# Performance work log

Hardware: AMD Instinct MI355X
Metric: run time of the kernel (lower is better)

The kernel has to match this reference:

```python
import math
import jax, jax.numpy as jnp
import numpy as np

K = 1.0            # Lorentz manifold curvature k
B, S = 4, 2048     # batch, seq_len
IN, H, OUT = 512, 8, 64   # in_channels, num_heads, out_channels (space dim; head_dim = OUT+1)


def setup_inputs() -> dict:
    key = jax.random.key(0)
    ks = jax.random.split(key, 8)
    std = 1.0 / math.sqrt(IN)
    return {
        "query_input": jax.random.normal(ks[0], (B, S, IN), jnp.float32),
        "source_input": jax.random.normal(ks[1], (B, S, IN), jnp.float32),
        # per-head HypLinear weights stacked on a leading head axis: [H, OUT, IN]
        "Wq_w": jax.random.normal(ks[2], (H, OUT, IN), jnp.float32) * std,
        "Wq_b": jnp.zeros((H, OUT), jnp.float32),
        "Wk_w": jax.random.normal(ks[3], (H, OUT, IN), jnp.float32) * std,
        "Wk_b": jnp.zeros((H, OUT), jnp.float32),
        "Wv_w": jax.random.normal(ks[4], (H, OUT, IN), jnp.float32) * std,
        "Wv_b": jnp.zeros((H, OUT), jnp.float32),
        "scale": jnp.array([math.sqrt(OUT)], jnp.float32),  # nn.Parameter([sqrt(out_channels)])
        "bias": jnp.zeros((), jnp.float32),                 # nn.Parameter(zeros(()))
    }


def hyp_linear(x, w, b):
    # HypLinear: linear map to space part, recompute Lorentz time coord sqrt(||x_s||^2 + k)
    sp = jnp.einsum('bsi,hoi->bsho', x, w) + b            # [B,S,H,OUT]
    t = jnp.sqrt(jnp.sum(sp * sp, axis=-1, keepdims=True) + K)
    return jnp.concatenate([t, sp], axis=-1)              # [B,S,H,OUT+1]


def reference(query_input, source_input, Wq_w, Wq_b, Wk_w, Wk_b, Wv_w, Wv_b, scale, bias):
    q = hyp_linear(query_input, Wq_w, Wq_b)   # [B,S,H,D], D = OUT+1
    k = hyp_linear(source_input, Wk_w, Wk_b)
    v = hyp_linear(source_input, Wv_w, Wv_b)

    # Lorentzian cinner: <x,y>_L = -x0*y0 + <x_s, y_s>
    sgn = jnp.concatenate([-jnp.ones((1,), q.dtype), jnp.ones((OUT,), q.dtype)])
    att = jnp.einsum('bqhd,bkhd->bhqk', q * sgn, k)       # [B,H,S,S]
    att = (2.0 + 2.0 * att) / scale[0] + bias

    causal = jnp.triu(jnp.full((S, S), -1e9, q.dtype), 1)  # causal mask (additive)
    att = jax.nn.softmax(att + causal, axis=-1)

    ctx = jnp.einsum('bhqk,bkhd->bqhd', att, v)           # [B,S,H,D]

    # manifold.mid_point over the heads axis (dim=-2)
    ave = jnp.mean(ctx, axis=2)                           # [B,S,D]
    inner = -ave[..., :1] ** 2 + jnp.sum(ave[..., 1:] ** 2, axis=-1, keepdims=True)
    denom = jnp.sqrt(jnp.maximum(jnp.abs(-inner), 1e-8))
    return math.sqrt(K) * ave / denom                     # [B,S,D]
```

## Files before the change

kernel.cpp:

```cpp
#include <hip/hip_runtime.h>

#define BATCH 4
#define SEQ   2048
#define INC   512
#define NH    8
#define OUTC  64
#define DD    65
#define NROW  (BATCH * NH * SEQ)

typedef float f32x4 __attribute__((ext_vector_type(4)));
typedef short short8 __attribute__((ext_vector_type(8)));
typedef short short4v __attribute__((ext_vector_type(4)));
typedef unsigned int uint2v __attribute__((ext_vector_type(2)));
typedef unsigned short us;

static __device__ __forceinline__ us f2b(float f) {
  unsigned int u = __float_as_uint(f);
  u = (u + 0x7FFFu + ((u >> 16) & 1u)) >> 16;
  return (us)u;
}
static __device__ __forceinline__ float b2f(us h) {
  return __uint_as_float(((unsigned int)h) << 16);
}
static __device__ __forceinline__ unsigned int pk2(float lo, float hi) {
  unsigned int r;
  asm("v_cvt_pk_bf16_f32 %0, %1, %2" : "=v"(r) : "v"(lo), "v"(hi));
  return r;
}

#define GLDS(g, l) __builtin_amdgcn_global_load_lds( \
    (const __attribute__((address_space(1))) void*)(g), \
    (__attribute__((address_space(3))) void*)(l), 16, 0, 0)
#define SB() __builtin_amdgcn_sched_barrier(0)

__global__ __launch_bounds__(256) void tobf16_kernel(
    const float* __restrict__ Xq, const float* __restrict__ Xs,
    const float* __restrict__ Wq, const float* __restrict__ Wk,
    const float* __restrict__ Wv,
    us* __restrict__ dXq, us* __restrict__ dXs,
    us* __restrict__ dWq, us* __restrict__ dWk, us* __restrict__ dWv)
{
  const int which = blockIdx.y;
  const float* src;
  us* dst;
  int n;
  switch (which) {
    case 0: src = Xq; dst = dXq; n = BATCH * SEQ * INC; break;
    case 1: src = Xs; dst = dXs; n = BATCH * SEQ * INC; break;
    case 2: src = Wq; dst = dWq; n = NH * OUTC * INC; break;
    case 3: src = Wk; dst = dWk; n = NH * OUTC * INC; break;
    default: src = Wv; dst = dWv; n = NH * OUTC * INC; break;
  }
  for (long i = (long)blockIdx.x * 256 + threadIdx.x; i * 4 < n;
       i += (long)gridDim.x * 256) {
    f32x4 v = *(const f32x4*)(src + i * 4);
    short4v o;
    o[0] = (short)f2b(v[0]); o[1] = (short)f2b(v[1]);
    o[2] = (short)f2b(v[2]); o[3] = (short)f2b(v[3]);
    *(short4v*)(dst + i * 4) = o;
  }
}

__global__ __launch_bounds__(256) void proj_kernel(
    const us* __restrict__ Xqb, const us* __restrict__ Xsb,
    const us* __restrict__ Wqb, const us* __restrict__ Wkb, const us* __restrict__ Wvb,
    const float* __restrict__ Bq, const float* __restrict__ Bk, const float* __restrict__ Bv,
    const float* __restrict__ scale_p,
    us* __restrict__ qs, unsigned int* __restrict__ qta,
    us* __restrict__ ks, unsigned int* __restrict__ kta,
    us* __restrict__ vs, us* __restrict__ vtc)
{
  const int which = blockIdx.z;
  const us* X = (which == 0) ? Xqb : Xsb;
  const us* W = (which == 0) ? Wqb : (which == 1 ? Wkb : Wvb);
  const float* Bb = (which == 0) ? Bq : (which == 1 ? Bk : Bv);
  us* outs = (which == 0) ? qs : (which == 1 ? ks : vs);
  const float al2 = (2.0f / scale_p[0]) * 1.44269504088896f;
  const float oscale = (which == 0) ? al2 : 1.0f;

  const int lin = blockIdx.x;
  const int h   = (lin >> 3) & 7;
  const int m0  = (((lin >> 6) << 3) | (lin & 7)) * 64;
  const int n0  = h * 64;

  __shared__ alignas(16) us lX[2][64 * 64];
  __shared__ alignas(16) us lW[2][64 * 64];

  const int tid  = threadIdx.x;
  const int lane = tid & 63;
  const int wave = tid >> 6;
  const int arow = lane & 15;
  const int agrp = lane >> 4;
  const int rl   = lane >> 3;
  const int chx  = ((lane & 7) ^ rl) * 8;
  const int r0   = wave * 8 + rl;
  const int r1   = r0 + 32;

#define PSTAGE(buf, k0) do { \
    GLDS(X + (size_t)(m0 + r0) * INC + (k0) + chx, &lX[buf][wave * 512]); \
    GLDS(X + (size_t)(m0 + r1) * INC + (k0) + chx, &lX[buf][2048 + wave * 512]); \
    GLDS(W + (size_t)(n0 + r0) * INC + (k0) + chx, &lW[buf][wave * 512]); \
    GLDS(W + (size_t)(n0 + r1) * INC + (k0) + chx, &lW[buf][2048 + wave * 512]); \
  } while (0)

  f32x4 acc[4] = {};
  PSTAGE(0, 0);

  for (int kk = 0; kk < 8; ++kk) {
    const int cur = kk & 1;
    if (kk < 7) {
      PSTAGE(cur ^ 1, (kk + 1) * 64);
      asm volatile("s_waitcnt vmcnt(4)");
    } else {
      asm volatile("s_waitcnt vmcnt(0)");
    }
    __builtin_amdgcn_s_barrier();
#pragma unroll
    for (int kc = 0; kc < 2; ++kc) {
      short8 af = *(const short8*)&lX[cur][(wave * 16 + arow) * 64 + (((kc * 4 + agrp) ^ (arow & 7)) * 8)];
#pragma unroll
      for (int c = 0; c < 4; ++c) {
        short8 bf = *(const short8*)&lW[cur][(c * 16 + arow) * 64 + (((kc * 4 + agrp) ^ (arow & 7)) * 8)];
        acc[c] = __builtin_amdgcn_mfma_f32_16x16x32_bf16(af, bf, acc[c], 0, 0, 0);
      }
    }
    __builtin_amdgcn_s_barrier();
  }

  float bcol[4];
#pragma unroll
  for (int c = 0; c < 4; ++c) bcol[c] = Bb[n0 + c * 16 + arow];
#pragma unroll
  for (int r = 0; r < 4; ++r) {
    float s2 = 0.f;
#pragma unroll
    for (int c = 0; c < 4; ++c) {
      float v = acc[c][r] + bcol[c];
      acc[c][r] = v;
      s2 += v * v;
    }
    s2 += __shfl_xor(s2, 1); s2 += __shfl_xor(s2, 2);
    s2 += __shfl_xor(s2, 4); s2 += __shfl_xor(s2, 8);
    float tv = sqrtf(s2 + 1.0f);
    int gs = m0 + wave * 16 + agrp * 4 + r;
    int bi = gs >> 11, si = gs & (SEQ - 1);
    size_t rowbase = (size_t)(bi * NH + h) * SEQ + si;
    size_t obase = rowbase * 64;
#pragma unroll
    for (int c = 0; c < 4; ++c) outs[obase + c * 16 + arow] = f2b(oscale * acc[c][r]);
    if (arow == 0) {
      if (which == 0) {
        float st = al2 * tv;
        us qh = f2b(st);
        us ql = f2b(st - b2f(qh));
        qta[rowbase] = (unsigned int)qh | ((unsigned int)ql << 16);
      } else {
        us th = f2b(tv);
        us tl = f2b(tv - b2f(th));
        if (which == 1) {
          kta[rowbase] = (unsigned int)(us)(th ^ 0x8000)
                       | ((unsigned int)(us)(tl ^ 0x8000) << 16);
        } else {
          vtc[rowbase] = th;
          vtc[NROW + rowbase] = tl;
        }
      }
    }
  }
}

__global__ __launch_bounds__(256) void transpose_v_kernel(
    const us* __restrict__ vs, us* __restrict__ vT)
{
  const int bh = blockIdx.y;
  const int s0 = blockIdx.x * 64;
  __shared__ us lT[64 * 80];
  const int tid = threadIdx.x;
#pragma unroll
  for (int u0 = 0; u0 < 2; ++u0) {
    int u = tid + u0 * 256;
    int row = u >> 3, ch = u & 7;
    short8 v = *(const short8*)&vs[((size_t)bh * SEQ + s0 + row) * 64 + ch * 8];
    *(short8*)&lT[row * 80 + ch * 8] = v;
  }
  __syncthreads();
#pragma unroll
  for (int u0 = 0; u0 < 2; ++u0) {
    int u = tid + u0 * 256;
    int o = u >> 3, sc = u & 7;
    short8 w;
#pragma unroll
    for (int j = 0; j < 8; ++j) w[j] = lT[(sc * 8 + j) * 80 + o];
    *(short8*)&vT[((size_t)bh * 64 + o) * SEQ + s0 + sc * 8] = w;
  }
}

__global__ __launch_bounds__(512) void attn_kernel(
    const us* __restrict__ qs, const unsigned int* __restrict__ qta,
    const us* __restrict__ ks, const unsigned int* __restrict__ kta,
    const us* __restrict__ vT, const us* __restrict__ vtc,
    float* __restrict__ part)
{
  const int f = blockIdx.x;
  const int xcd = f & 7, idx = f >> 3;
  const int bh = xcd * 4 + (idx / 24);
  const int inner = idx % 24;
  const int x = inner / 3;
  const int s = inner % 3;
  const int n0 = 2 * x + 2;
  const int n1 = 32 - 2 * x;

  __shared__ alignas(16) us lK[2][64 * 64];
  __shared__ alignas(16) us lV[2][64 * 64];
  __shared__ alignas(16) us lP[8][16 * 40];

  const int tid  = threadIdx.x;
  const int lane = tid & 63;
  const int wave = tid >> 6;
  const int arow = lane & 15;
  const int agrp = lane >> 4;

  const size_t bhbase = (size_t)bh * SEQ;
  const us* kgp = ks + bhbase * 64;
  const us* vgp = vT + (size_t)bh * 64 * SEQ;
  const unsigned int* ktp = kta + bhbase;
  const us* vtp = vtc + (size_t)(arow & 1) * NROW + bhbase;

  const int rl   = lane >> 3;
  const int chx  = ((lane & 7) ^ rl) * 8;
  const int dsl0 = (agrp ^ (arow & 7)) * 8;
  const int dsl1 = ((4 + agrp) ^ (arow & 7)) * 8;
  us* myP = &lP[wave][0];
  const int pw0 = arow * 40 + agrp * 4;
  const int prd = arow * 40 + agrp * 8;

#define ASTAGE(buf, t64) do { \
    const int kk = (t64) * 64; \
    GLDS(kgp + (size_t)(kk + wave * 8 + rl) * 64 + chx, &lK[buf][wave * 512]); \
    GLDS(vgp + (size_t)(wave * 8 + rl) * SEQ + kk + chx, &lV[buf][wave * 512]); \
  } while (0)

  short8 ones8, zero8 = {};
#pragma unroll
  for (int j = 0; j < 8; ++j) ones8[j] = (short)0x3F80;

  for (int seg = 0; seg < 2; ++seg) {
    const int qT = seg ? (15 - x) : x;
    int lo, hi;
    if (seg == 0) { lo = min(12 * s, n0);          hi = min(12 * s + 12, n0); }
    else          { lo = max(12 * s - n0, 0);      hi = min(12 * s + 12 - n0, n1); }
    const int nt = hi - lo;
    if (nt <= 0) continue;

    const int wq = qT * 128 + wave * 16 + arow;
    f32x4 acc[5] = {};

    const us* qp = qs + (bhbase + wq) * 64;
    short8 qf0 = *(const short8*)(qp + agrp * 8);
    short8 qf1 = *(const short8*)(qp + 32 + agrp * 8);
    unsigned int qw = qta[bhbase + wq];
    short8 qf2 = {};
    if (agrp == 0) {
      qf2[0] = (short)(qw & 0xFFFFu);
      qf2[1] = (short)(qw & 0xFFFFu);
      qf2[2] = (short)(qw >> 16);
    }

    unsigned int ka[4];
    short8 va0, va1;
    {
      const int kk = lo * 64;
#pragma unroll
      for (int c = 0; c < 4; ++c) ka[c] = ktp[kk + c * 16 + arow];
      va0 = *(const short8*)(vtp + kk + agrp * 8);
      va1 = *(const short8*)(vtp + kk + 32 + agrp * 8);
    }
    SB();
    ASTAGE(0, lo);
    SB();

    for (int it = 0; it < nt; ++it) {
      const int t = lo + it;
      const int cur = it & 1;
      if (it < nt - 1) {
        ASTAGE(cur ^ 1, t + 1);
        SB();
        asm volatile("s_waitcnt vmcnt(2)");
      } else {
        SB();
        asm volatile("s_waitcnt vmcnt(0)");
      }
      SB();
      __builtin_amdgcn_s_barrier();

      const us* Kb = lK[cur];
      const us* Vb = lV[cur];

      f32x4 sS[4] = {};
      __builtin_amdgcn_s_setprio(1);
#pragma unroll
      for (int c = 0; c < 4; ++c) {
        short8 kf = *(const short8*)&Kb[(c * 16 + arow) * 64 + dsl0];
        sS[c] = __builtin_amdgcn_mfma_f32_16x16x32_bf16(kf, qf0, sS[c], 0, 0, 0);
      }
#pragma unroll
      for (int c = 0; c < 4; ++c) {
        short8 kf = *(const short8*)&Kb[(c * 16 + arow) * 64 + dsl1];
        sS[c] = __builtin_amdgcn_mfma_f32_16x16x32_bf16(kf, qf1, sS[c], 0, 0, 0);
      }
#pragma unroll
      for (int c = 0; c < 4; ++c) {
        short8 kf2 = {};
        if (agrp == 0) {
          unsigned int w0 = ka[c];
          kf2[0] = (short)(w0 & 0xFFFFu);
          kf2[1] = (short)(w0 >> 16);
          kf2[2] = (short)(w0 & 0xFFFFu);
        }
        sS[c] = __builtin_amdgcn_mfma_f32_16x16x32_bf16(kf2, qf2, sS[c], 0, 0, 0);
      }
      __builtin_amdgcn_s_setprio(0);

#pragma unroll
      for (int c = 0; c < 4; ++c)
#pragma unroll
        for (int r = 0; r < 4; ++r)
          sS[c][r] = exp2f(sS[c][r]);
      if (t >= 2 * qT) {
        const int kb = t * 64;
#pragma unroll
        for (int c = 0; c < 4; ++c)
#pragma unroll
          for (int r = 0; r < 4; ++r)
            if (kb + c * 16 + agrp * 4 + r > wq) sS[c][r] = 0.f;
      }

      {
        uint2v w;
        w[0] = pk2(sS[0][0], sS[0][1]); w[1] = pk2(sS[0][2], sS[0][3]);
        *(uint2v*)&myP[pw0] = w;
        w[0] = pk2(sS[1][0], sS[1][1]); w[1] = pk2(sS[1][2], sS[1][3]);
        *(uint2v*)&myP[pw0 + 16] = w;
        short8 pf = *(const short8*)&myP[prd];
        __builtin_amdgcn_s_setprio(1);
#pragma unroll
        for (int dc = 0; dc < 4; ++dc) {
          short8 vf = *(const short8*)&Vb[(dc * 16 + arow) * 64 + dsl0];
          acc[dc] = __builtin_amdgcn_mfma_f32_16x16x32_bf16(pf, vf, acc[dc], 0, 0, 0);
        }
        short8 vf4 = (arow < 2) ? va0 : ((arow == 2) ? ones8 : zero8);
        acc[4] = __builtin_amdgcn_mfma_f32_16x16x32_bf16(pf, vf4, acc[4], 0, 0, 0);
        __builtin_amdgcn_s_setprio(0);
      }
      {
        uint2v w;
        w[0] = pk2(sS[2][0], sS[2][1]); w[1] = pk2(sS[2][2], sS[2][3]);
        *(uint2v*)&myP[pw0] = w;
        w[0] = pk2(sS[3][0], sS[3][1]); w[1] = pk2(sS[3][2], sS[3][3]);
        *(uint2v*)&myP[pw0 + 16] = w;
        short8 pf = *(const short8*)&myP[prd];
        __builtin_amdgcn_s_setprio(1);
#pragma unroll
        for (int dc = 0; dc < 4; ++dc) {
          short8 vf = *(const short8*)&Vb[(dc * 16 + arow) * 64 + dsl1];
          acc[dc] = __builtin_amdgcn_mfma_f32_16x16x32_bf16(pf, vf, acc[dc], 0, 0, 0);
        }
        short8 vf4 = (arow < 2) ? va1 : ((arow == 2) ? ones8 : zero8);
        acc[4] = __builtin_amdgcn_mfma_f32_16x16x32_bf16(pf, vf4, acc[4], 0, 0, 0);
        __builtin_amdgcn_s_setprio(0);
      }

      SB();
      if (it + 1 < nt) {
        const int kk = (t + 1) * 64;
#pragma unroll
        for (int c = 0; c < 4; ++c) ka[c] = ktp[kk + c * 16 + arow];
        va0 = *(const short8*)(vtp + kk + agrp * 8);
        va1 = *(const short8*)(vtp + kk + 32 + agrp * 8);
      }
      SB();
      __builtin_amdgcn_s_barrier();
    }

    const size_t pb = ((size_t)(bh * 16 + qT) * 3 + s) * 128;
#pragma unroll
    for (int r = 0; r < 4; ++r) {
      float t0 = __shfl(acc[4][r], (agrp << 4) | 0);
      float t1 = __shfl(acc[4][r], (agrp << 4) | 1);
      float ls = __shfl(acc[4][r], (agrp << 4) | 2);
      size_t rp = (pb + wave * 16 + agrp * 4 + r) * 68;
#pragma unroll
      for (int dc = 0; dc < 4; ++dc)
        part[rp + dc * 16 + arow] = acc[dc][r];
      if (arow == 0) {
        part[rp + 64] = t0 + t1;
        part[rp + 65] = ls;
      }
    }
  }
}

__global__ __launch_bounds__(256) void finalize_kernel(
    const float* __restrict__ part, float* __restrict__ out)
{
  const int tid  = threadIdx.x;
  const int lane = tid & 63;
  const int gw = blockIdx.x * 4 + (tid >> 6);
  const int b = gw >> 11, si = gw & (SEQ - 1);
  const int qT = si >> 7, row = si & 127;

  const bool v0 = (qT <= 7) || (qT >= 11);
  const bool v1 = (qT >= 6);
  const bool v2 = (qT >= 8);

  float vsum = 0.f, tsum = 0.f;
#pragma unroll
  for (int h = 0; h < NH; ++h) {
    const size_t tb = ((size_t)(b * NH + h) * 16 + qT) * 3;
    float Ah = 0.f, Th = 0.f, Lh = 0.f;
    if (v0) {
      size_t rb = ((tb + 0) * 128 + row) * 68;
      Ah += part[rb + lane]; Th += part[rb + 64]; Lh += part[rb + 65];
    }
    if (v1) {
      size_t rb = ((tb + 1) * 128 + row) * 68;
      Ah += part[rb + lane]; Th += part[rb + 64]; Lh += part[rb + 65];
    }
    if (v2) {
      size_t rb = ((tb + 2) * 128 + row) * 68;
      Ah += part[rb + lane]; Th += part[rb + 64]; Lh += part[rb + 65];
    }
    float inv = 1.0f / Lh;
    vsum = fmaf(Ah, inv, vsum);
    tsum = fmaf(Th, inv, tsum);
  }
  float ave  = vsum * 0.125f;
  float tave = tsum * 0.125f;
  float contrib = ave * ave;
  if (lane == 0) contrib -= tave * tave;
  contrib += __shfl_xor(contrib, 1);
  contrib += __shfl_xor(contrib, 2);
  contrib += __shfl_xor(contrib, 4);
  contrib += __shfl_xor(contrib, 8);
  contrib += __shfl_xor(contrib, 16);
  contrib += __shfl_xor(contrib, 32);
  float denom = sqrtf(fmaxf(fabsf(contrib), 1e-8f));
  size_t ob = ((size_t)b * SEQ + si) * (size_t)DD;
  out[ob + 1 + lane] = ave / denom;
  if (lane == 0) out[ob] = tave / denom;
}

extern "C" void kernel_launch(void* const* d_in, const int* in_sizes, int n_in,
                              void* d_out, int out_size, void* d_ws, size_t ws_size,
                              hipStream_t stream) {
  const float* Xq  = (const float*)d_in[0];
  const float* Xs  = (const float*)d_in[1];
  const float* Wq  = (const float*)d_in[2];
  const float* Bq  = (const float*)d_in[3];
  const float* Wk  = (const float*)d_in[4];
  const float* Bk  = (const float*)d_in[5];
  const float* Wv  = (const float*)d_in[6];
  const float* Bv  = (const float*)d_in[7];
  const float* scale = (const float*)d_in[8];
  float* out = (float*)d_out;

  char* p = (char*)d_ws;

  float* part = (float*)p;
  us* Xqb   = (us*)p;
  us* Xsb   = (us*)(p + 16777216);
  us* Wqb16 = (us*)(p + 33554432);
  us* Wkb16 = (us*)(p + 34078720);
  us* Wvb16 = (us*)(p + 34603008);
  us* vsb   = (us*)(p + 35651584);
  p += (size_t)32 * 16 * 3 * 128 * 68 * 4;
  us* qsb = (us*)p; p += (size_t)NROW * 64 * 2;
  us* ksb = (us*)p; p += (size_t)NROW * 64 * 2;
  us* vTb = (us*)p; p += (size_t)NROW * 64 * 2;
  unsigned int* qtaw = (unsigned int*)p; p += (size_t)NROW * 4;
  unsigned int* ktaw = (unsigned int*)p; p += (size_t)NROW * 4;
  us* vtcw = (us*)p; p += (size_t)NROW * 2 * 2;

  tobf16_kernel<<<dim3(1024, 5), 256, 0, stream>>>(
      Xq, Xs, Wq, Wk, Wv, Xqb, Xsb, Wqb16, Wkb16, Wvb16);
  proj_kernel<<<dim3(1024, 1, 3), 256, 0, stream>>>(
      Xqb, Xsb, Wqb16, Wkb16, Wvb16, Bq, Bk, Bv, scale,
      qsb, qtaw, ksb, ktaw, vsb, vtcw);
  transpose_v_kernel<<<dim3(SEQ / 64, BATCH * NH), 256, 0, stream>>>(vsb, vTb);
  attn_kernel<<<dim3(768), 512, 0, stream>>>(
      qsb, qtaw, ksb, ktaw, vTb, vtcw, part);
  finalize_kernel<<<(BATCH * SEQ) / 4, 256, 0, stream>>>(part, out);
}
```

Baseline: 100.4 us.

## Fuse V transpose into projection kernel and store attention partials as bf16

The V projection blocks now stage their output tile in shared memory and write V already transposed, which removes the separate transpose kernel launch and the round trip of V through global memory. The attention partial context vectors are stored as bf16 with a 72-element stride, keeping the time and sum fields as fp32. This cuts the bytes written by the attention kernel and read by finalize. Storing partials in bf16 loses precision before the normalisation and cross-split sum.

Result: faster. 96.30 us, median of 2 (-4.1%).

```diff
diff --git a/kernel.cpp b/kernel.cpp
--- a/kernel.cpp
+++ b/kernel.cpp
@@ -7,6 +7,7 @@
 #define OUTC  64
 #define DD    65
 #define NROW  (BATCH * NH * SEQ)
+#define PSTRIDE 72
 
 typedef float f32x4 __attribute__((ext_vector_type(4)));
 typedef short short8 __attribute__((ext_vector_type(8)));
@@ -68,13 +69,12 @@
     const float* __restrict__ scale_p,
     us* __restrict__ qs, unsigned int* __restrict__ qta,
     us* __restrict__ ks, unsigned int* __restrict__ kta,
-    us* __restrict__ vs, us* __restrict__ vtc)
+    us* __restrict__ vT, us* __restrict__ vtc)
 {
   const int which = blockIdx.z;
   const us* X = (which == 0) ? Xqb : Xsb;
   const us* W = (which == 0) ? Wqb : (which == 1 ? Wkb : Wvb);
   const float* Bb = (which == 0) ? Bq : (which == 1 ? Bk : Bv);
-  us* outs = (which == 0) ? qs : (which == 1 ? ks : vs);
   const float al2 = (2.0f / scale_p[0]) * 1.44269504088896f;
   const float oscale = (which == 0) ? al2 : 1.0f;
 
@@ -83,8 +83,8 @@
   const int m0  = (((lin >> 6) << 3) | (lin & 7)) * 64;
   const int n0  = h * 64;
 
-  __shared__ alignas(16) us lX[2][64 * 64];
-  __shared__ alignas(16) us lW[2][64 * 64];
+  __shared__ alignas(16) us lXf[2 * 64 * 64];
+  __shared__ alignas(16) us lWf[2 * 64 * 64];
 
   const int tid  = threadIdx.x;
   const int lane = tid & 63;
@@ -97,10 +97,10 @@
   const int r1   = r0 + 32;
 
 #define PSTAGE(buf, k0) do { \
-    GLDS(X + (size_t)(m0 + r0) * INC + (k0) + chx, &lX[buf][wave * 512]); \
-    GLDS(X + (size_t)(m0 + r1) * INC + (k0) + chx, &lX[buf][2048 + wave * 512]); \
-    GLDS(W + (size_t)(n0 + r0) * INC + (k0) + chx, &lW[buf][wave * 512]); \
-    GLDS(W + (size_t)(n0 + r1) * INC + (k0) + chx, &lW[buf][2048 + wave * 512]); \
+    GLDS(X + (size_t)(m0 + r0) * INC + (k0) + chx, &lXf[(buf) * 4096 + wave * 512]); \
+    GLDS(X + (size_t)(m0 + r1) * INC + (k0) + chx, &lXf[(buf) * 4096 + 2048 + wave * 512]); \
+    GLDS(W + (size_t)(n0 + r0) * INC + (k0) + chx, &lWf[(buf) * 4096 + wave * 512]); \
+    GLDS(W + (size_t)(n0 + r1) * INC + (k0) + chx, &lWf[(buf) * 4096 + 2048 + wave * 512]); \
   } while (0)
 
   f32x4 acc[4] = {};
@@ -117,10 +117,10 @@
     __builtin_amdgcn_s_barrier();
 #pragma unroll
     for (int kc = 0; kc < 2; ++kc) {
-      short8 af = *(const short8*)&lX[cur][(wave * 16 + arow) * 64 + (((kc * 4 + agrp) ^ (arow & 7)) * 8)];
+      short8 af = *(const short8*)&lXf[cur * 4096 + (wave * 16 + arow) * 64 + (((kc * 4 + agrp) ^ (arow & 7)) * 8)];
 #pragma unroll
       for (int c = 0; c < 4; ++c) {
-        short8 bf = *(const short8*)&lW[cur][(c * 16 + arow) * 64 + (((kc * 4 + agrp) ^ (arow & 7)) * 8)];
+        short8 bf = *(const short8*)&lWf[cur * 4096 + (c * 16 + arow) * 64 + (((kc * 4 + agrp) ^ (arow & 7)) * 8)];
         acc[c] = __builtin_amdgcn_mfma_f32_16x16x32_bf16(af, bf, acc[c], 0, 0, 0);
       }
     }
@@ -130,6 +130,9 @@
   float bcol[4];
 #pragma unroll
   for (int c = 0; c < 4; ++c) bcol[c] = Bb[n0 + c * 16 + arow];
+
+  us* lT = &lXf[0];
+
 #pragma unroll
   for (int r = 0; r < 4; ++r) {
     float s2 = 0.f;
@@ -145,53 +148,49 @@
     int gs = m0 + wave * 16 + agrp * 4 + r;
     int bi = gs >> 11, si = gs & (SEQ - 1);
     size_t rowbase = (size_t)(bi * NH + h) * SEQ + si;
-    size_t obase = rowbase * 64;
-#pragma unroll
-    for (int c = 0; c < 4; ++c) outs[obase + c * 16 + arow] = f2b(oscale * acc[c][r]);
-    if (arow == 0) {
-      if (which == 0) {
-        float st = al2 * tv;
-        us qh = f2b(st);
-        us ql = f2b(st - b2f(qh));
-        qta[rowbase] = (unsigned int)qh | ((unsigned int)ql << 16);
-      } else {
+    if (which == 2) {
+      int lrow = wave * 16 + agrp * 4 + r;
+#pragma unroll
+      for (int c = 0; c < 4; ++c)
+        lT[lrow * PSTRIDE + c * 16 + arow] = f2b(acc[c][r]);
+      if (arow == 0) {
         us th = f2b(tv);
         us tl = f2b(tv - b2f(th));
-        if (which == 1) {
-          kta[rowbase] = (unsigned int)(us)(th ^ 0x8000)
-                       | ((unsigned int)(us)(tl ^ 0x8000) << 16);
+        vtc[rowbase] = th;
+        vtc[NROW + rowbase] = tl;
+      }
+    } else {
+      us* outs = (which == 0) ? qs : ks;
+      size_t obase = rowbase * 64;
+#pragma unroll
+      for (int c = 0; c < 4; ++c) outs[obase + c * 16 + arow] = f2b(oscale * acc[c][r]);
+      if (arow == 0) {
+        if (which == 0) {
+          float st = al2 * tv;
+          us qh = f2b(st);
+          us ql = f2b(st - b2f(qh));
+          qta[rowbase] = (unsigned int)qh | ((unsigned int)ql << 16);
         } else {
-          vtc[rowbase] = th;
-          vtc[NROW + rowbase] = tl;
+          kta[rowbase] = (unsigned int)(us)(f2b(tv) ^ 0x8000)
+                       | ((unsigned int)(us)(f2b(tv - b2f(f2b(tv))) ^ 0x8000) << 16);
         }
       }
     }
   }
-}
-
-__global__ __launch_bounds__(256) void transpose_v_kernel(
-    const us* __restrict__ vs, us* __restrict__ vT)
-{
-  const int bh = blockIdx.y;
-  const int s0 = blockIdx.x * 64;
-  __shared__ us lT[64 * 80];
-  const int tid = threadIdx.x;
-#pragma unroll
-  for (int u0 = 0; u0 < 2; ++u0) {
-    int u = tid + u0 * 256;
-    int row = u >> 3, ch = u & 7;
-    short8 v = *(const short8*)&vs[((size_t)bh * SEQ + s0 + row) * 64 + ch * 8];
-    *(short8*)&lT[row * 80 + ch * 8] = v;
-  }
-  __syncthreads();
-#pragma unroll
-  for (int u0 = 0; u0 < 2; ++u0) {
-    int u = tid + u0 * 256;
-    int o = u >> 3, sc = u & 7;
-    short8 w;
-#pragma unroll
-    for (int j = 0; j < 8; ++j) w[j] = lT[(sc * 8 + j) * 80 + o];
-    *(short8*)&vT[((size_t)bh * 64 + o) * SEQ + s0 + sc * 8] = w;
+
+  if (which == 2) {
+    __syncthreads();
+    const int bi = m0 >> 11, si0 = m0 & (SEQ - 1);
+    us* vbase = vT + ((size_t)(bi * NH + h) * 64) * SEQ + si0;
+#pragma unroll
+    for (int u0 = 0; u0 < 2; ++u0) {
+      int u = tid + u0 * 256;
+      int o = u >> 3, jc = u & 7;
+      short8 w;
+#pragma unroll
+      for (int j = 0; j < 8; ++j) w[j] = (short)lT[(jc * 8 + j) * PSTRIDE + o];
+      *(short8*)(vbase + (size_t)o * SEQ + jc * 8) = w;
+    }
   }
 }
 
@@ -199,7 +198,7 @@
     const us* __restrict__ qs, const unsigned int* __restrict__ qta,
     const us* __restrict__ ks, const unsigned int* __restrict__ kta,
     const us* __restrict__ vT, const us* __restrict__ vtc,
-    float* __restrict__ part)
+    us* __restrict__ part)
 {
   const int f = blockIdx.x;
   const int xcd = f & 7, idx = f >> 3;
@@ -388,20 +387,21 @@
       float t0 = __shfl(acc[4][r], (agrp << 4) | 0);
       float t1 = __shfl(acc[4][r], (agrp << 4) | 1);
       float ls = __shfl(acc[4][r], (agrp << 4) | 2);
-      size_t rp = (pb + wave * 16 + agrp * 4 + r) * 68;
+      size_t rp = (pb + wave * 16 + agrp * 4 + r) * PSTRIDE;
 #pragma unroll
       for (int dc = 0; dc < 4; ++dc)
-        part[rp + dc * 16 + arow] = acc[dc][r];
+        part[rp + dc * 16 + arow] = f2b(acc[dc][r]);
       if (arow == 0) {
-        part[rp + 64] = t0 + t1;
-        part[rp + 65] = ls;
+        float* fp = (float*)(part + rp + 64);
+        fp[0] = t0 + t1;
+        fp[1] = ls;
       }
     }
   }
 }
 
 __global__ __launch_bounds__(256) void finalize_kernel(
-    const float* __restrict__ part, float* __restrict__ out)
+    const us* __restrict__ part, float* __restrict__ out)
 {
   const int tid  = threadIdx.x;
   const int lane = tid & 63;
@@ -419,16 +419,22 @@
     const size_t tb = ((size_t)(b * NH + h) * 16 + qT) * 3;
     float Ah = 0.f, Th = 0.f, Lh = 0.f;
     if (v0) {
-      size_t rb = ((tb + 0) * 128 + row) * 68;
-      Ah += part[rb + lane]; Th += part[rb + 64]; Lh += part[rb + 65];
+      size_t rb = ((tb + 0) * 128 + row) * PSTRIDE;
+      Ah += b2f(part[rb + lane]);
+      const float* fp = (const float*)(part + rb + 64);
+      Th += fp[0]; Lh += fp[1];
     }
     if (v1) {
-      size_t rb = ((tb + 1) * 128 + row) * 68;
-      Ah += part[rb + lane]; Th += part[rb + 64]; Lh += part[rb + 65];
+      size_t rb = ((tb + 1) * 128 + row) * PSTRIDE;
+      Ah += b2f(part[rb + lane]);
+      const float* fp = (const float*)(part + rb + 64);
+      Th += fp[0]; Lh += fp[1];
     }
     if (v2) {
-      size_t rb = ((tb + 2) * 128 + row) * 68;
-      Ah += part[rb + lane]; Th += part[rb + 64]; Lh += part[rb + 65];
+      size_t rb = ((tb + 2) * 128 + row) * PSTRIDE;
+      Ah += b2f(part[rb + lane]);
+      const float* fp = (const float*)(part + rb + 64);
+      Th += fp[0]; Lh += fp[1];
     }
     float inv = 1.0f / Lh;
     vsum = fmaf(Ah, inv, vsum);
@@ -466,14 +472,13 @@
 
   char* p = (char*)d_ws;
 
-  float* part = (float*)p;
+  us* partw = (us*)p;
   us* Xqb   = (us*)p;
   us* Xsb   = (us*)(p + 16777216);
   us* Wqb16 = (us*)(p + 33554432);
   us* Wkb16 = (us*)(p + 34078720);
   us* Wvb16 = (us*)(p + 34603008);
-  us* vsb   = (us*)(p + 35651584);
-  p += (size_t)32 * 16 * 3 * 128 * 68 * 4;
+  p += 35651584;
   us* qsb = (us*)p; p += (size_t)NROW * 64 * 2;
   us* ksb = (us*)p; p += (size_t)NROW * 64 * 2;
   us* vTb = (us*)p; p += (size_t)NROW * 64 * 2;
@@ -485,9 +490,8 @@
       Xq, Xs, Wq, Wk, Wv, Xqb, Xsb, Wqb16, Wkb16, Wvb16);
   proj_kernel<<<dim3(1024, 1, 3), 256, 0, stream>>>(
       Xqb, Xsb, Wqb16, Wkb16, Wvb16, Bq, Bk, Bv, scale,
-      qsb, qtaw, ksb, ktaw, vsb, vtcw);
-  transpose_v_kernel<<<dim3(SEQ / 64, BATCH * NH), 256, 0, stream>>>(vsb, vTb);
+      qsb, qtaw, ksb, ktaw, vTb, vtcw);
   attn_kernel<<<dim3(768), 512, 0, stream>>>(
-      qsb, qtaw, ksb, ktaw, vTb, vtcw, part);
-  finalize_kernel<<<(BATCH * SEQ) / 4, 256, 0, stream>>>(part, out);
-}
+      qsb, qtaw, ksb, ktaw, vTb, vtcw, partw);
+  finalize_kernel<<<(BATCH * SEQ) / 4, 256, 0, stream>>>(partw, out);
+}
```
